# Performance work log

Measured on AMD Instinct MI355X. Metric: run time of the kernel, lower is better.

The kernel has to match this reference:

```python
import jax, jax.numpy as jnp
import numpy as np
import math

H = 1024  # hidden_dim
NH = 16   # num_heads
HD = H // NH  # head_dim = 64
B, S, C = 2, 2048, 256  # batch, seq_len, cond_len
EPS = 1e-5


def layernorm(x, g, b):
    m = jnp.mean(x, axis=-1, keepdims=True)
    v = jnp.var(x, axis=-1, keepdims=True)
    return (x - m) * jax.lax.rsqrt(v + EPS) * g + b


def apply_rope(x, freqs):
    # x: [b, s, h, d], freqs broadcastable to [b, s, h, d//2]
    cos, sin = jnp.cos(freqs), jnp.sin(freqs)
    x1, x2 = jnp.split(x, 2, axis=-1)
    return jnp.concatenate([x1 * cos - x2 * sin, x2 * cos + x1 * sin], axis=-1)


def setup_inputs() -> dict:
    key = jax.random.key(0)
    ks = jax.random.split(key, 16)
    sc = 0.02
    x = jax.random.normal(ks[0], (B, S, H), jnp.float32)
    # rope freqs: positions * inv_freq over half head dim
    inv_freq = 1.0 / (10000.0 ** (jnp.arange(HD // 2, dtype=jnp.float32) / (HD // 2)))
    rope_freqs = (jnp.arange(S, dtype=jnp.float32)[:, None] * inv_freq[None, :]).reshape(S, 1, HD // 2)
    # causal additive mask [1,1,S,S]
    causal = jnp.tril(jnp.ones((S, S), dtype=bool))
    attention_mask = jnp.where(causal, 0.0, -1e9).astype(jnp.float32)[None, None]
    conditioning = jax.random.normal(ks[1], (B, C, H), jnp.float32)
    conditioning_mask = jnp.zeros((B, 1, 1, C), jnp.float32)
    params = dict(
        ln1_g=jnp.ones((H,)), ln1_b=jnp.zeros((H,)),
        ln2_g=jnp.ones((H,)), ln2_b=jnp.zeros((H,)),
        lnc_g=jnp.ones((H,)), lnc_b=jnp.zeros((H,)),
        w_qkv=jax.random.normal(ks[2], (H, 3 * H)) * sc,
        w_out=jax.random.normal(ks[3], (H, H)) * sc, b_out=jnp.zeros((H,)),
        w_cq=jax.random.normal(ks[4], (H, H)) * sc,
        w_ckv=jax.random.normal(ks[5], (H, 2 * H)) * sc,
        w_cout=jax.random.normal(ks[6], (H, H)) * sc, b_cout=jnp.zeros((H,)),
        w_ff1=jax.random.normal(ks[7], (H, 4 * H)) * sc, b_ff1=jnp.zeros((4 * H,)),
        w_ff2=jax.random.normal(ks[8], (4 * H, H)) * sc, b_ff2=jnp.zeros((H,)),
    )
    return dict(x=x, rope_freqs=rope_freqs, attention_mask=attention_mask,
                conditioning=conditioning, conditioning_mask=conditioning_mask, **params)


def reference(x, rope_freqs, attention_mask, conditioning, conditioning_mask,
              ln1_g, ln1_b, ln2_g, ln2_b, lnc_g, lnc_b,
              w_qkv, w_out, b_out, w_cq, w_ckv, w_cout, b_cout,
              w_ff1, b_ff1, w_ff2, b_ff2):
    scale = 1.0 / math.sqrt(HD)
    # --- causal self-attention ---
    residual = x
    h = layernorm(x, ln1_g, ln1_b)
    qkv = h @ w_qkv  # [b,s,3H]
    q, k, v = jnp.split(qkv, 3, axis=-1)
    q = q.reshape(B, S, NH, HD)
    k = k.reshape(B, S, NH, HD)
    v = v.reshape(B, S, NH, HD)
    q = apply_rope(q, rope_freqs)
    k = apply_rope(k, rope_freqs)
    scores = jnp.einsum('bqhd,bkhd->bhqk', q, k) * scale + attention_mask
    attn = jax.nn.softmax(scores, axis=-1)
    out = jnp.einsum('bhqk,bkhd->bqhd', attn, v).reshape(B, S, H)
    x = residual + out @ w_out + b_out
    # --- cross-attention ---
    residual = x
    h = layernorm(x, lnc_g, lnc_b)
    q = (h @ w_cq).reshape(B, S, NH, HD)
    kv = conditioning @ w_ckv
    k, v = jnp.split(kv, 2, axis=-1)
    k = k.reshape(B, C, NH, HD)
    v = v.reshape(B, C, NH, HD)
    scores = jnp.einsum('bqhd,bkhd->bhqk', q, k) * scale + conditioning_mask
    attn = jax.nn.softmax(scores, axis=-1)
    out = jnp.einsum('bhqk,bkhd->bqhd', attn, v).reshape(B, S, H)
    x = residual + out @ w_cout + b_cout
    # --- FFN ---
    residual = x
    h = layernorm(x, ln2_g, ln2_b)
    h = jax.nn.gelu(h @ w_ff1 + b_ff1, approximate=False)
    x = residual + h @ w_ff2 + b_ff2
    return x
```

## Files before the change

kernel.cpp:

```cpp
#include <hip/hip_runtime.h>

#define HDIM   1024
#define NHEADS 16
#define HEADD  64
#define BATCH  2
#define SEQ    2048
#define CLEN   256
#define NROWS  (BATCH*SEQ)
#define SCALE  0.125f
#define LOG2E  1.44269504088896f

typedef __bf16 bf16x8 __attribute__((ext_vector_type(8)));
typedef float  f32x4  __attribute__((ext_vector_type(4)));

__device__ __forceinline__ unsigned short f2bf(float f) {
  union { __bf16 b; unsigned short u; } x;
  x.b = (__bf16)f;
  return x.u;
}
__device__ __forceinline__ float bf2f(unsigned short u) {
  union { unsigned int u; float f; } x; x.u = ((unsigned int)u) << 16;
  return x.f;
}

__device__ __forceinline__ void gl2lds16(const unsigned short* g, unsigned short* l) {
  __builtin_amdgcn_global_load_lds(
      (const __attribute__((address_space(1))) unsigned int*)g,
      (__attribute__((address_space(3))) unsigned int*)l, 16, 0, 0);
}

template<int VM> __device__ __forceinline__ void wait_vm_barrier() {
  if constexpr (VM == 0)      asm volatile("s_waitcnt vmcnt(0)\n\ts_barrier" ::: "memory");
  else if constexpr (VM == 2) asm volatile("s_waitcnt vmcnt(2)\n\ts_barrier" ::: "memory");
  else if constexpr (VM == 3) asm volatile("s_waitcnt vmcnt(3)\n\ts_barrier" ::: "memory");
  else if constexpr (VM == 4) asm volatile("s_waitcnt vmcnt(4)\n\ts_barrier" ::: "memory");
  else                        asm volatile("s_waitcnt vmcnt(6)\n\ts_barrier" ::: "memory");
}
__device__ __forceinline__ void bar_only() { asm volatile("s_barrier" ::: "memory"); }

struct CastTab { const float* s[8]; unsigned short* d[8]; };

__global__ __launch_bounds__(256)
void cast_fused(CastTab tab) {
  __shared__ float t[64][68];
  const int bid = blockIdx.x;
  const int tid = threadIdx.x;
  int w, base, K, N;
  if      (bid < 768)  { w = 0; base = 0;    K = 1024; N = 3072; }
  else if (bid < 1024) { w = 1; base = 768;  K = 1024; N = 1024; }
  else if (bid < 1280) { w = 2; base = 1024; K = 1024; N = 1024; }
  else if (bid < 1792) { w = 3; base = 1280; K = 1024; N = 2048; }
  else if (bid < 2048) { w = 4; base = 1792; K = 1024; N = 1024; }
  else if (bid < 3072) { w = 5; base = 2048; K = 1024; N = 4096; }
  else if (bid < 4096) { w = 6; base = 3072; K = 4096; N = 1024; }
  else                 { w = 7; base = 4096; K = 0;    N = 0;    }
  if (w == 7) {
    const float* in = tab.s[7];
    unsigned short* out = tab.d[7];
    int i = (bid - base) * 256 + tid;
    float4 a = ((const float4*)in)[2 * i], bq = ((const float4*)in)[2 * i + 1];
    unsigned short us[8] = { f2bf(a.x),  f2bf(a.y),  f2bf(a.z),  f2bf(a.w),
                             f2bf(bq.x), f2bf(bq.y), f2bf(bq.z), f2bf(bq.w) };
    ((uint4*)out)[i] = *(uint4*)us;
    return;
  }
  const float* in = tab.s[w];
  unsigned short* out = tab.d[w];
  const int lb = bid - base;
  const int tilesX = N >> 6;
  const int bx = lb % tilesX, by = lb / tilesX;
  const int kb = by * 64, nb = bx * 64;
  const int r = tid >> 4, c = (tid & 15) * 4;
#pragma unroll
  for (int i = 0; i < 4; ++i) {
    float4 v = *(const float4*)(in + (size_t)(kb + r + i * 16) * N + nb + c);
    t[r + i * 16][c]     = v.x;
    t[r + i * 16][c + 1] = v.y;
    t[r + i * 16][c + 2] = v.z;
    t[r + i * 16][c + 3] = v.w;
  }
  __syncthreads();
  const int nr = tid >> 3, kc = (tid & 7) * 8;
#pragma unroll
  for (int i = 0; i < 2; ++i) {
    unsigned short us[8];
#pragma unroll
    for (int j = 0; j < 8; ++j) us[j] = f2bf(t[kc + j][nr + i * 32]);
    *(uint4*)(out + (size_t)(nb + nr + i * 32) * K + kb + kc) = *(uint4*)us;
  }
}

__global__ __launch_bounds__(256)
void vtrans_kernel(const unsigned short* __restrict__ in, int str, int voff, int rows,
                   unsigned short* __restrict__ out) {
  __shared__ unsigned short t[64][72];
  const int h = blockIdx.y & (NHEADS - 1), b = blockIdx.y >> 4;
  const int s0 = blockIdx.x * 64;
  const int tid = threadIdx.x;
  const int r = tid >> 2, c = (tid & 3) * 16;
  const unsigned short* src = in + (size_t)(b * rows + s0 + r) * str + voff + h * 64 + c;
  *(uint4*)(&t[r][c])     = *(const uint4*)(src);
  *(uint4*)(&t[r][c + 8]) = *(const uint4*)(src + 8);
  __syncthreads();
  const int d = tid >> 2, sc = (tid & 3) * 16;
  unsigned short tmp[16];
#pragma unroll
  for (int i = 0; i < 16; ++i) tmp[i] = t[sc + i][d];
  unsigned short* dst = out + ((size_t)(b * NHEADS + h) * 64 + d) * rows + s0 + sc;
  *(uint4*)(dst)     = *(uint4*)(tmp);
  *(uint4*)(dst + 8) = *(uint4*)(tmp + 8);
}

__global__ __launch_bounds__(256)
void layernorm_kernel(const float* __restrict__ x, const float* __restrict__ g,
                      const float* __restrict__ b, unsigned short* __restrict__ out) {
  int row = blockIdx.x;
  const float4 v = ((const float4*)(x + (size_t)row * HDIM))[threadIdx.x];
  float s  = v.x + v.y + v.z + v.w;
  float sq = v.x*v.x + v.y*v.y + v.z*v.z + v.w*v.w;
  for (int o = 32; o; o >>= 1) { s += __shfl_xor(s, o); sq += __shfl_xor(sq, o); }
  __shared__ float rs[4], rq[4];
  int wave = threadIdx.x >> 6;
  if ((threadIdx.x & 63) == 0) { rs[wave] = s; rq[wave] = sq; }
  __syncthreads();
  s  = rs[0] + rs[1] + rs[2] + rs[3];
  sq = rq[0] + rq[1] + rq[2] + rq[3];
  float mean = s * (1.f/HDIM);
  float var  = sq * (1.f/HDIM) - mean*mean;
  float rstd = rsqrtf(var + 1e-5f);
  float4 gg = ((const float4*)g)[threadIdx.x];
  float4 bb = ((const float4*)b)[threadIdx.x];
  ushort4 o;
  o.x = f2bf((v.x - mean) * rstd * gg.x + bb.x);
  o.y = f2bf((v.y - mean) * rstd * gg.y + bb.y);
  o.z = f2bf((v.z - mean) * rstd * gg.z + bb.z);
  o.w = f2bf((v.w - mean) * rstd * gg.w + bb.w);
  ((ushort4*)(out + (size_t)row * HDIM))[threadIdx.x] = o;
}

template<int TBM, int TBN, int DEPTH, bool BIAS, bool RES, bool GELU_, bool OUTBF>
__global__ __launch_bounds__(512)
void gemm_bt(const unsigned short* __restrict__ A, const unsigned short* __restrict__ Bt,
             const float* __restrict__ bias, const float* __restrict__ res,
             void* __restrict__ out, int M, int N, int K) {
  constexpr int MR = TBM / 32;
  constexpr int NR = TBN / 64;
  constexpr int AIS = TBM / 64;
  constexpr int BIS = TBN / 64;
  constexpr int LOADS = AIS + BIS;
  constexpr int NBUF = DEPTH + 1;
  __shared__ unsigned short Al[NBUF][TBM * 64];
  __shared__ unsigned short Bl[NBUF][TBN * 64];
  const int tid  = threadIdx.x;
  const int wave = tid >> 6, lane = tid & 63;
  const int wr = wave >> 2, wc = wave & 3;
  const int nwg = gridDim.x * gridDim.y;
  int lin = blockIdx.y * gridDim.x + blockIdx.x;
  lin = (lin & 7) * (nwg >> 3) + (lin >> 3);
  const int m0 = (lin / gridDim.x) * TBM, n0 = (lin % gridDim.x) * TBN;
  const int lrow = lane & 15, hi = lane >> 4;
  const int rx = lrow & 7;

  f32x4 acc[MR][NR] = {};

  const int trow = tid >> 3, pslot = tid & 7;
  const int lcol = (pslot ^ (trow & 7)) * 8;
  const unsigned short* ga = A  + (size_t)(m0 + trow) * K + lcol;
  const unsigned short* gb = Bt + (size_t)(n0 + trow) * K + lcol;
  const int ldst = trow * 64 + pslot * 8;
  const int nt = K >> 6;

  auto stage = [&](int buf, int t) {
    const int k = t << 6;
#pragma unroll
    for (int i = 0; i < AIS; ++i)
      gl2lds16(ga + (size_t)i * 64 * K + k, Al[buf] + ldst + i * 64 * 64);
#pragma unroll
    for (int i = 0; i < BIS; ++i)
      gl2lds16(gb + (size_t)i * 64 * K + k, Bl[buf] + ldst + i * 64 * 64);
  };
  auto compute = [&](int c) {
#pragma unroll
    for (int kk = 0; kk < 2; ++kk) {
      const int cslot = ((kk << 2) | hi);
      const int coff  = (cslot ^ rx) * 8;
      bf16x8 af[MR], bfr[NR];
#pragma unroll
      for (int m = 0; m < MR; ++m)
        af[m] = *(const bf16x8*)(Al[c] + (wr*(TBM/2) + m*16 + lrow) * 64 + coff);
#pragma unroll
      for (int n = 0; n < NR; ++n)
        bfr[n] = *(const bf16x8*)(Bl[c] + (wc*(TBN/4) + n*16 + lrow) * 64 + coff);
#pragma unroll
      for (int m = 0; m < MR; ++m)
#pragma unroll
        for (int n = 0; n < NR; ++n)
          acc[m][n] = __builtin_amdgcn_mfma_f32_16x16x32_bf16(af[m], bfr[n], acc[m][n], 0, 0, 0);
    }
  };

  stage(0, 0);
  if constexpr (DEPTH == 2) stage(1, 1);
  int cur = 0;
  for (int t = 0; t < nt - DEPTH; ++t) {
    int nb = cur + DEPTH; if (nb >= NBUF) nb -= NBUF;
    stage(nb, t + DEPTH);
    wait_vm_barrier<DEPTH * LOADS>();
    compute(cur);
    bar_only();
    cur = (cur + 1 == NBUF) ? 0 : cur + 1;
  }
  if constexpr (DEPTH == 2) {
    wait_vm_barrier<LOADS>();
    compute(cur);
    bar_only();
    cur = (cur + 1 == NBUF) ? 0 : cur + 1;
  }
  wait_vm_barrier<0>();
  compute(cur);

#pragma unroll
  for (int m = 0; m < MR; ++m)
#pragma unroll
    for (int n = 0; n < NR; ++n)
#pragma unroll
      for (int r = 0; r < 4; ++r) {
        int row = m0 + wr*(TBM/2) + m*16 + hi * 4 + r;
        int col = n0 + wc*(TBN/4) + n*16 + lrow;
        float v = acc[m][n][r];
        if (BIAS)  v += bias[col];
        if (GELU_) v = 0.5f * v * (1.0f + erff(v * 0.70710678118654752f));
        if (RES)   v += res[(size_t)row * N + col];
        if (OUTBF) ((unsigned short*)out)[(size_t)row * N + col] = f2bf(v);
        else       ((float*)out)[(size_t)row * N + col] = v;
      }
}

__global__ void rope_kernel(unsigned short* __restrict__ qkv, const float* __restrict__ freqs) {
  int idx = blockIdx.x * 256 + threadIdx.x;
  int d = idx & 31;
  int h = (idx >> 5) & 15;
  int row = idx >> 9;
  int s = row & (SEQ - 1);
  float f = freqs[s * 32 + d];
  float sn, cs;
  sincosf(f, &sn, &cs);
  size_t base = (size_t)row * 3072 + h * 64 + d;
  float x1 = bf2f(qkv[base]), x2 = bf2f(qkv[base + 32]);
  qkv[base]      = f2bf(x1 * cs - x2 * sn);
  qkv[base + 32] = f2bf(x2 * cs + x1 * sn);
  float y1 = bf2f(qkv[base + 1024]), y2 = bf2f(qkv[base + 1024 + 32]);
  qkv[base + 1024]      = f2bf(y1 * cs - y2 * sn);
  qkv[base + 1024 + 32] = f2bf(y2 * cs + y1 * sn);
}

__global__ __launch_bounds__(512)
void flash_attn_causal8(const unsigned short* __restrict__ qp, int qstr,
                        const unsigned short* __restrict__ kp, int kstr,
                        const unsigned short* __restrict__ vt,
                        unsigned short* __restrict__ outp) {
  __shared__ unsigned short Kl[2][64 * 64];
  __shared__ unsigned short Vl[2][64 * 64];
  __shared__ unsigned short Pl[8][16][72];

  const int id = blockIdx.y * gridDim.x + blockIdx.x;
  const int bh = (id & 7) * 4 + ((id >> 3) & 3);
  const int qpair = id >> 5;
  const int h = bh & (NHEADS - 1), b = bh >> 4;

  const int tid = threadIdx.x;
  const int wave = tid >> 6, lane = tid & 63;
  const int grp = wave >> 2, w4 = wave & 3;
  const int lo = lane & 15, hi = lane >> 4;
  const int NQB = SEQ / 64;
  const float SC2 = SCALE * LOG2E;
  float* mb = (float*)&Pl[0][0][0];

  bf16x8 onesf;
#pragma unroll
  for (int j = 0; j < 8; ++j) onesf[j] = (__bf16)1.0f;

  const unsigned short* vbase = vt + (size_t)(b * NHEADS + h) * 64 * SEQ;
  const int g256 = tid & 255;
  const int trow = g256 >> 3, pslot = g256 & 7;
  const int lcol = (pslot ^ (trow & 7)) * 8;
  const int ldst = g256 * 8;
  const int x7 = lo & 7;
  const int c0 = (hi ^ x7) * 8, c1 = ((hi + 4) ^ x7) * 8;

  for (int pass = 0; pass < 2; ++pass) {
    const int qblk = pass == 0 ? qpair : NQB - 1 - qpair;
    const int q0 = qblk * 64;
    const int qw = q0 + w4 * 16;

    bf16x8 qf[2];
    {
      const unsigned short* qb = qp + (size_t)(b * SEQ + qw + lo) * qstr + h * 64 + hi * 8;
      qf[0] = *(const bf16x8*)(qb);
      qf[1] = *(const bf16x8*)(qb + 32);
#pragma unroll
      for (int j = 0; j < 8; ++j) {
        qf[0][j] = (__bf16)((float)qf[0][j] * SC2);
        qf[1][j] = (__bf16)((float)qf[1][j] * SC2);
      }
    }

    f32x4 o_acc[4] = {};
    f32x4 l_acc = {};
    float mrow[4];
#pragma unroll
    for (int r = 0; r < 4; ++r) mrow[r] = -1e30f;

    const int T = qblk + 1;
    const int iters = (T + 1) >> 1;
    for (int it = 0; it < iters; ++it) {
      const int t = 2 * it + grp;
      const bool act = t < T;
      const int j0 = t * 64;
      if (act) {
        const unsigned short* ks = kp + (size_t)(b * SEQ + j0 + trow) * kstr + h * 64 + lcol;
        const unsigned short* vs = vbase + (size_t)trow * SEQ + j0 + lcol;
        gl2lds16(ks, Kl[grp] + ldst);
        gl2lds16(ks + (size_t)32 * kstr, Kl[grp] + ldst + 32 * 64);
        gl2lds16(vs, Vl[grp] + ldst);
        gl2lds16(vs + (size_t)32 * SEQ, Vl[grp] + ldst + 32 * 64);
      }
      __syncthreads();
      if (act) {
        const unsigned short* Kc = Kl[grp];
        const unsigned short* Vc = Vl[grp];
        f32x4 s[4] = {};
#pragma unroll
        for (int n = 0; n < 4; ++n) {
          bf16x8 b0 = *(const bf16x8*)(Kc + (n * 16 + lo) * 64 + c0);
          bf16x8 b1 = *(const bf16x8*)(Kc + (n * 16 + lo) * 64 + c1);
          s[n] = __builtin_amdgcn_mfma_f32_16x16x32_bf16(qf[0], b0, s[n], 0, 0, 0);
          s[n] = __builtin_amdgcn_mfma_f32_16x16x32_bf16(qf[1], b1, s[n], 0, 0, 0);
        }
        if (t == T - 1) {
#pragma unroll
          for (int n = 0; n < 4; ++n)
#pragma unroll
            for (int r = 0; r < 4; ++r)
              if (j0 + n * 16 + lo > qw + hi * 4 + r) s[n][r] = -1e30f;
        }
        float pr[4][4];
#pragma unroll
        for (int r = 0; r < 4; ++r) {
          float mx = fmaxf(fmaxf(s[0][r], s[1][r]), fmaxf(s[2][r], s[3][r]));
          mx = fmaxf(mx, __shfl_xor(mx, 1));
          mx = fmaxf(mx, __shfl_xor(mx, 2));
          mx = fmaxf(mx, __shfl_xor(mx, 4));
          mx = fmaxf(mx, __shfl_xor(mx, 8));
          const float mnew = fmaxf(mrow[r], mx);
          const float corr = exp2f(mrow[r] - mnew);
          mrow[r] = mnew;
          l_acc[r] *= corr;
#pragma unroll
          for (int n = 0; n < 4; ++n)
            pr[n][r] = exp2f(s[n][r] - mnew);
#pragma unroll
          for (int n2 = 0; n2 < 4; ++n2) o_acc[n2][r] *= corr;
        }
#pragma unroll
        for (int n = 0; n < 4; ++n)
#pragma unroll
          for (int r = 0; r < 4; ++r)
            Pl[wave][hi * 4 + r][n * 16 + lo] = f2bf(pr[n][r]);

        bf16x8 pa0 = *(const bf16x8*)(&Pl[wave][lo][hi * 8]);
        bf16x8 pa1 = *(const bf16x8*)(&Pl[wave][lo][32 + hi * 8]);
        l_acc = __builtin_amdgcn_mfma_f32_16x16x32_bf16(pa0, onesf, l_acc, 0, 0, 0);
        l_acc = __builtin_amdgcn_mfma_f32_16x16x32_bf16(pa1, onesf, l_acc, 0, 0, 0);
#pragma unroll
        for (int n = 0; n < 4; ++n) {
          bf16x8 vb0 = *(const bf16x8*)(Vc + (n * 16 + lo) * 64 + c0);
          bf16x8 vb1 = *(const bf16x8*)(Vc + (n * 16 + lo) * 64 + c1);
          o_acc[n] = __builtin_amdgcn_mfma_f32_16x16x32_bf16(pa0, vb0, o_acc[n], 0, 0, 0);
          o_acc[n] = __builtin_amdgcn_mfma_f32_16x16x32_bf16(pa1, vb1, o_acc[n], 0, 0, 0);
        }
      }
      __syncthreads();
    }

    unsigned short* ob = outp + (size_t)(b * SEQ + qw) * HDIM + h * 64;
#pragma unroll
    for (int half = 0; half < 2; ++half) {
      __syncthreads();
      if (grp == 1) {
        float* dst = mb + (w4 * 64 + lane) * 13;
#pragma unroll
        for (int rr = 0; rr < 2; ++rr) {
          int r = half * 2 + rr;
          dst[rr * 6]     = mrow[r];
          dst[rr * 6 + 1] = l_acc[r];
#pragma unroll
          for (int n = 0; n < 4; ++n) dst[rr * 6 + 2 + n] = o_acc[n][r];
        }
      }
      __syncthreads();
      if (grp == 0) {
        const float* s1 = mb + (w4 * 64 + lane) * 13;
#pragma unroll
        for (int rr = 0; rr < 2; ++rr) {
          int r = half * 2 + rr;
          float m1 = s1[rr * 6], l1 = s1[rr * 6 + 1];
          float M  = fmaxf(mrow[r], m1);
          float c0f = exp2f(mrow[r] - M), c1f = exp2f(m1 - M);
          float inv = 1.f / (l_acc[r] * c0f + l1 * c1f);
#pragma unroll
          for (int n = 0; n < 4; ++n) {
            float o = o_acc[n][r] * c0f + s1[rr * 6 + 2 + n] * c1f;
            ob[(size_t)(hi * 4 + r) * HDIM + n * 16 + lo] = f2bf(o * inv);
          }
        }
      }
    }
    __syncthreads();
  }
}

__global__ __launch_bounds__(256)
void flash_attn_cross(const unsigned short* __restrict__ qp, int qstr,
                      const unsigned short* __restrict__ kp, int kstr,
                      const unsigned short* __restrict__ vt,
                      int kvrows,
                      unsigned short* __restrict__ outp) {
  __shared__ unsigned short Kl[2][64 * 64];
  __shared__ unsigned short Vl[2][64 * 64];
  __shared__ unsigned short Pl[4][16][72];

  const int id = blockIdx.y * gridDim.x + blockIdx.x;
  const int bh = (id & 7) * 4 + ((id >> 3) & 3);
  const int qblk = id >> 5;
  const int h = bh & (NHEADS - 1), b = bh >> 4;

  const int tid = threadIdx.x;
  const int wave = tid >> 6, lane = tid & 63;
  const int lo = lane & 15, hi = lane >> 4;
  const float SC2 = SCALE * LOG2E;

  bf16x8 onesf;
#pragma unroll
  for (int j = 0; j < 8; ++j) onesf[j] = (__bf16)1.0f;

  const unsigned short* vbase = vt + (size_t)(b * NHEADS + h) * 64 * kvrows;
  const int trow = tid >> 3, pslot = tid & 7;
  const int lcol = (pslot ^ (trow & 7)) * 8;
  const int ldst = tid * 8;
  const int x7 = lo & 7;
  const int c0 = (hi ^ x7) * 8, c1 = ((hi + 4) ^ x7) * 8;

  const int qw = qblk * 64 + wave * 16;

  bf16x8 qf[2];
  {
    const unsigned short* qb = qp + (size_t)(b * SEQ + qw + lo) * qstr + h * 64 + hi * 8;
    qf[0] = *(const bf16x8*)(qb);
    qf[1] = *(const bf16x8*)(qb + 32);
#pragma unroll
    for (int j = 0; j < 8; ++j) {
      qf[0][j] = (__bf16)((float)qf[0][j] * SC2);
      qf[1][j] = (__bf16)((float)qf[1][j] * SC2);
    }
  }

  f32x4 o_acc[4] = {};
  f32x4 l_acc = {};
  float mrow[4];
#pragma unroll
  for (int r = 0; r < 4; ++r) mrow[r] = -1e30f;

  auto stageKV = [&](int buf, int t) {
    const int j = t * 64;
    const unsigned short* ks = kp + (size_t)(b * kvrows + j + trow) * kstr + h * 64 + lcol;
    const unsigned short* vs = vbase + (size_t)trow * kvrows + j + lcol;
    gl2lds16(ks, Kl[buf] + ldst);
    gl2lds16(ks + (size_t)32 * kstr, Kl[buf] + ldst + 32 * 64);
    gl2lds16(vs, Vl[buf] + ldst);
    gl2lds16(vs + (size_t)32 * kvrows, Vl[buf] + ldst + 32 * 64);
  };
  auto computeTile = [&](int c) {
    const unsigned short* Kc = Kl[c];
    const unsigned short* Vc = Vl[c];
    f32x4 s[4] = {};
#pragma unroll
    for (int n = 0; n < 4; ++n) {
      bf16x8 b0 = *(const bf16x8*)(Kc + (n * 16 + lo) * 64 + c0);
      bf16x8 b1 = *(const bf16x8*)(Kc + (n * 16 + lo) * 64 + c1);
      s[n] = __builtin_amdgcn_mfma_f32_16x16x32_bf16(qf[0], b0, s[n], 0, 0, 0);
      s[n] = __builtin_amdgcn_mfma_f32_16x16x32_bf16(qf[1], b1, s[n], 0, 0, 0);
    }
    float pr[4][4];
#pragma unroll
    for (int r = 0; r < 4; ++r) {
      float mx = fmaxf(fmaxf(s[0][r], s[1][r]), fmaxf(s[2][r], s[3][r]));
      mx = fmaxf(mx, __shfl_xor(mx, 1));
      mx = fmaxf(mx, __shfl_xor(mx, 2));
      mx = fmaxf(mx, __shfl_xor(mx, 4));
      mx = fmaxf(mx, __shfl_xor(mx, 8));
      const float mnew = fmaxf(mrow[r], mx);
      const float corr = exp2f(mrow[r] - mnew);
      mrow[r] = mnew;
      l_acc[r] *= corr;
#pragma unroll
      for (int n = 0; n < 4; ++n)
        pr[n][r] = exp2f(s[n][r] - mnew);
#pragma unroll
      for (int n2 = 0; n2 < 4; ++n2) o_acc[n2][r] *= corr;
    }
#pragma unroll
    for (int n = 0; n < 4; ++n)
#pragma unroll
      for (int r = 0; r < 4; ++r)
        Pl[wave][hi * 4 + r][n * 16 + lo] = f2bf(pr[n][r]);
    bf16x8 pa0 = *(const bf16x8*)(&Pl[wave][lo][hi * 8]);
    bf16x8 pa1 = *(const bf16x8*)(&Pl[wave][lo][32 + hi * 8]);
    l_acc = __builtin_amdgcn_mfma_f32_16x16x32_bf16(pa0, onesf, l_acc, 0, 0, 0);
    l_acc = __builtin_amdgcn_mfma_f32_16x16x32_bf16(pa1, onesf, l_acc, 0, 0, 0);
#pragma unroll
    for (int n = 0; n < 4; ++n) {
      bf16x8 vb0 = *(const bf16x8*)(Vc + (n * 16 + lo) * 64 + c0);
      bf16x8 vb1 = *(const bf16x8*)(Vc + (n * 16 + lo) * 64 + c1);
      o_acc[n] = __builtin_amdgcn_mfma_f32_16x16x32_bf16(pa0, vb0, o_acc[n], 0, 0, 0);
      o_acc[n] = __builtin_amdgcn_mfma_f32_16x16x32_bf16(pa1, vb1, o_acc[n], 0, 0, 0);
    }
  };

  const int T = kvrows / 64;
  stageKV(0, 0);
  int cur = 0;
  for (int t = 0; t < T - 1; ++t) {
    stageKV(cur ^ 1, t + 1);
    wait_vm_barrier<4>();
    computeTile(cur);
    bar_only();
    cur ^= 1;
  }
  wait_vm_barrier<0>();
  computeTile(cur);

  unsigned short* ob = outp + (size_t)(b * SEQ + qw) * HDIM + h * 64;
#pragma unroll
  for (int r = 0; r < 4; ++r) {
    const float inv = 1.f / l_acc[r];
#pragma unroll
    for (int n = 0; n < 4; ++n)
      ob[(size_t)(hi * 4 + r) * HDIM + n * 16 + lo] = f2bf(o_acc[n][r] * inv);
  }
}

extern "C" void kernel_launch(void* const* d_in, const int* in_sizes, int n_in,
                              void* d_out, int out_size, void* d_ws, size_t ws_size,
                              hipStream_t stream) {
  const float* x      = (const float*)d_in[0];
  const float* rfreq  = (const float*)d_in[1];
  const float* cond   = (const float*)d_in[3];
  const float* ln1_g  = (const float*)d_in[5];
  const float* ln1_b  = (const float*)d_in[6];
  const float* ln2_g  = (const float*)d_in[7];
  const float* ln2_b  = (const float*)d_in[8];
  const float* lnc_g  = (const float*)d_in[9];
  const float* lnc_b  = (const float*)d_in[10];
  const float* w_qkv  = (const float*)d_in[11];
  const float* w_out  = (const float*)d_in[12];
  const float* b_out  = (const float*)d_in[13];
  const float* w_cq   = (const float*)d_in[14];
  const float* w_ckv  = (const float*)d_in[15];
  const float* w_cout = (const float*)d_in[16];
  const float* b_cout = (const float*)d_in[17];
  const float* w_ff1  = (const float*)d_in[18];
  const float* b_ff1  = (const float*)d_in[19];
  const float* w_ff2  = (const float*)d_in[20];
  const float* b_ff2  = (const float*)d_in[21];

  char* ws = (char*)d_ws;
  size_t off = 0;
  auto alloc = [&](size_t bytes) { size_t r = off; off += (bytes + 255) & ~(size_t)255; return r; };
  unsigned short* wt_qkv  = (unsigned short*)(ws + alloc((size_t)3072*1024*2));
  unsigned short* wt_out  = (unsigned short*)(ws + alloc((size_t)1024*1024*2));
  unsigned short* wt_cq   = (unsigned short*)(ws + alloc((size_t)1024*1024*2));
  unsigned short* wt_ckv  = (unsigned short*)(ws + alloc((size_t)2048*1024*2));
  unsigned short* wt_cout = (unsigned short*)(ws + alloc((size_t)1024*1024*2));
  unsigned short* wt_ff1  = (unsigned short*)(ws + alloc((size_t)4096*1024*2));
  unsigned short* wt_ff2  = (unsigned short*)(ws + alloc((size_t)1024*4096*2));
  unsigned short* condb   = (unsigned short*)(ws + alloc((size_t)512*1024*2));
  unsigned short* hbuf    = (unsigned short*)(ws + alloc((size_t)NROWS*1024*2));
  unsigned short* big     = (unsigned short*)(ws + alloc((size_t)NROWS*4096*2));
  unsigned short* attnb   = (unsigned short*)(ws + alloc((size_t)NROWS*1024*2));
  float*          x1      = (float*)(ws + alloc((size_t)NROWS*1024*4));
  unsigned short* kvc     = (unsigned short*)(ws + alloc((size_t)512*2048*2));
  unsigned short* vts     = (unsigned short*)(ws + alloc((size_t)BATCH*NHEADS*64*SEQ*2));
  unsigned short* vtc     = (unsigned short*)(ws + alloc((size_t)BATCH*NHEADS*64*CLEN*2));
  float*          outf    = (float*)d_out;

  CastTab tab;
  tab.s[0] = w_qkv;  tab.d[0] = wt_qkv;
  tab.s[1] = w_out;  tab.d[1] = wt_out;
  tab.s[2] = w_cq;   tab.d[2] = wt_cq;
  tab.s[3] = w_ckv;  tab.d[3] = wt_ckv;
  tab.s[4] = w_cout; tab.d[4] = wt_cout;
  tab.s[5] = w_ff1;  tab.d[5] = wt_ff1;
  tab.s[6] = w_ff2;  tab.d[6] = wt_ff2;
  tab.s[7] = cond;   tab.d[7] = condb;
  cast_fused<<<4352, 256, 0, stream>>>(tab);

  layernorm_kernel<<<NROWS, 256, 0, stream>>>(x, ln1_g, ln1_b, hbuf);
  gemm_bt<128,128,1,false,false,false,true><<<dim3(3072/128, NROWS/128), 512, 0, stream>>>(
      hbuf, wt_qkv, nullptr, nullptr, big, NROWS, 3072, 1024);
  rope_kernel<<<(NROWS*NHEADS*32)/256, 256, 0, stream>>>(big, rfreq);
  vtrans_kernel<<<dim3(SEQ/64, BATCH*NHEADS), 256, 0, stream>>>(big, 3072, 2048, SEQ, vts);
  flash_attn_causal8<<<dim3(SEQ/64/2, BATCH*NHEADS), 512, 0, stream>>>(
      big, 3072, big + 1024, 3072, vts, attnb);
  gemm_bt<128,64,2,true,true,false,false><<<dim3(1024/64, NROWS/128), 512, 0, stream>>>(
      attnb, wt_out, b_out, x, x1, NROWS, 1024, 1024);

  layernorm_kernel<<<NROWS, 256, 0, stream>>>(x1, lnc_g, lnc_b, hbuf);
  gemm_bt<128,64,2,false,false,false,true><<<dim3(1024/64, NROWS/128), 512, 0, stream>>>(
      hbuf, wt_cq, nullptr, nullptr, big, NROWS, 1024, 1024);
  gemm_bt<64,64,2,false,false,false,true><<<dim3(2048/64, 512/64), 512, 0, stream>>>(
      condb, wt_ckv, nullptr, nullptr, kvc, 512, 2048, 1024);
  vtrans_kernel<<<dim3(CLEN/64, BATCH*NHEADS), 256, 0, stream>>>(kvc, 2048, 1024, CLEN, vtc);
  flash_attn_cross<<<dim3(SEQ/64, BATCH*NHEADS), 256, 0, stream>>>(
      big, 1024, kvc, 2048, vtc, CLEN, attnb);
  gemm_bt<128,64,2,true,true,false,false><<<dim3(1024/64, NROWS/128), 512, 0, stream>>>(
      attnb, wt_cout, b_cout, x1, outf, NROWS, 1024, 1024);

  layernorm_kernel<<<NROWS, 256, 0, stream>>>(outf, ln2_g, ln2_b, hbuf);
  gemm_bt<128,128,1,true,false,true,true><<<dim3(4096/128, NROWS/128), 512, 0, stream>>>(
      hbuf, wt_ff1, b_ff1, nullptr, big, NROWS, 4096, 1024);
  gemm_bt<128,64,2,true,true,false,false><<<dim3(1024/64, NROWS/128), 512, 0, stream>>>(
      big, wt_ff2, b_ff2, outf, outf, NROWS, 1024, 4096);
}
```

Before: 316.3 us.

## Fuse Q RoPE into causal attention and store mid residual in bf16

The separate RoPE pass now rotates only K. The rotation of Q moves into the causal flash-attention kernel's Q load, using sincos on the frequency table. The intermediate residual after self-attention is stored as bf16 instead of fp32, with a new bf16 layernorm and a bf16-residual path in the GEMM epilogue. This is meant to cut global memory traffic in the rope, out-projection, layernorm and cout kernels. The cost is extra sincos work per attention block (done twice per block because of the two passes) and lower precision in the residual stream.

```diff
diff --git a/kernel.cpp b/kernel.cpp
--- a/kernel.cpp
+++ b/kernel.cpp
@@ -138,10 +138,38 @@
   ((ushort4*)(out + (size_t)row * HDIM))[threadIdx.x] = o;
 }
 
-template<int TBM, int TBN, int DEPTH, bool BIAS, bool RES, bool GELU_, bool OUTBF>
+__global__ __launch_bounds__(256)
+void layernorm_bf16_kernel(const unsigned short* __restrict__ x, const float* __restrict__ g,
+                           const float* __restrict__ b, unsigned short* __restrict__ out) {
+  int row = blockIdx.x;
+  ushort4 uv = ((const ushort4*)(x + (size_t)row * HDIM))[threadIdx.x];
+  float v0 = bf2f(uv.x), v1 = bf2f(uv.y), v2 = bf2f(uv.z), v3 = bf2f(uv.w);
+  float s  = v0 + v1 + v2 + v3;
+  float sq = v0*v0 + v1*v1 + v2*v2 + v3*v3;
+  for (int o = 32; o; o >>= 1) { s += __shfl_xor(s, o); sq += __shfl_xor(sq, o); }
+  __shared__ float rs[4], rq[4];
+  int wave = threadIdx.x >> 6;
+  if ((threadIdx.x & 63) == 0) { rs[wave] = s; rq[wave] = sq; }
+  __syncthreads();
+  s  = rs[0] + rs[1] + rs[2] + rs[3];
+  sq = rq[0] + rq[1] + rq[2] + rq[3];
+  float mean = s * (1.f/HDIM);
+  float var  = sq * (1.f/HDIM) - mean*mean;
+  float rstd = rsqrtf(var + 1e-5f);
+  float4 gg = ((const float4*)g)[threadIdx.x];
+  float4 bb = ((const float4*)b)[threadIdx.x];
+  ushort4 o;
+  o.x = f2bf((v0 - mean) * rstd * gg.x + bb.x);
+  o.y = f2bf((v1 - mean) * rstd * gg.y + bb.y);
+  o.z = f2bf((v2 - mean) * rstd * gg.z + bb.z);
+  o.w = f2bf((v3 - mean) * rstd * gg.w + bb.w);
+  ((ushort4*)(out + (size_t)row * HDIM))[threadIdx.x] = o;
+}
+
+template<int TBM, int TBN, int DEPTH, bool BIAS, bool RES, bool RESBF, bool GELU_, bool OUTBF>
 __global__ __launch_bounds__(512)
 void gemm_bt(const unsigned short* __restrict__ A, const unsigned short* __restrict__ Bt,
-             const float* __restrict__ bias, const float* __restrict__ res,
+             const float* __restrict__ bias, const void* __restrict__ res,
              void* __restrict__ out, int M, int N, int K) {
   constexpr int MR = TBM / 32;
   constexpr int NR = TBN / 64;
@@ -230,13 +258,16 @@
         float v = acc[m][n][r];
         if (BIAS)  v += bias[col];
         if (GELU_) v = 0.5f * v * (1.0f + erff(v * 0.70710678118654752f));
-        if (RES)   v += res[(size_t)row * N + col];
+        if (RES) {
+          if constexpr (RESBF) v += bf2f(((const unsigned short*)res)[(size_t)row * N + col]);
+          else                 v += ((const float*)res)[(size_t)row * N + col];
+        }
         if (OUTBF) ((unsigned short*)out)[(size_t)row * N + col] = f2bf(v);
         else       ((float*)out)[(size_t)row * N + col] = v;
       }
 }
 
-__global__ void rope_kernel(unsigned short* __restrict__ qkv, const float* __restrict__ freqs) {
+__global__ void rope_k_kernel(unsigned short* __restrict__ qkv, const float* __restrict__ freqs) {
   int idx = blockIdx.x * 256 + threadIdx.x;
   int d = idx & 31;
   int h = (idx >> 5) & 15;
@@ -245,19 +276,17 @@
   float f = freqs[s * 32 + d];
   float sn, cs;
   sincosf(f, &sn, &cs);
-  size_t base = (size_t)row * 3072 + h * 64 + d;
-  float x1 = bf2f(qkv[base]), x2 = bf2f(qkv[base + 32]);
-  qkv[base]      = f2bf(x1 * cs - x2 * sn);
-  qkv[base + 32] = f2bf(x2 * cs + x1 * sn);
-  float y1 = bf2f(qkv[base + 1024]), y2 = bf2f(qkv[base + 1024 + 32]);
-  qkv[base + 1024]      = f2bf(y1 * cs - y2 * sn);
-  qkv[base + 1024 + 32] = f2bf(y2 * cs + y1 * sn);
+  size_t base = (size_t)row * 3072 + h * 64 + d + 1024;
+  float y1 = bf2f(qkv[base]), y2 = bf2f(qkv[base + 32]);
+  qkv[base]      = f2bf(y1 * cs - y2 * sn);
+  qkv[base + 32] = f2bf(y2 * cs + y1 * sn);
 }
 
 __global__ __launch_bounds__(512)
 void flash_attn_causal8(const unsigned short* __restrict__ qp, int qstr,
                         const unsigned short* __restrict__ kp, int kstr,
                         const unsigned short* __restrict__ vt,
+                        const float* __restrict__ rfreq,
                         unsigned short* __restrict__ outp) {
   __shared__ unsigned short Kl[2][64 * 64];
   __shared__ unsigned short Vl[2][64 * 64];
@@ -298,10 +327,14 @@
       const unsigned short* qb = qp + (size_t)(b * SEQ + qw + lo) * qstr + h * 64 + hi * 8;
       qf[0] = *(const bf16x8*)(qb);
       qf[1] = *(const bf16x8*)(qb + 32);
+      const float* fr = rfreq + (size_t)(qw + lo) * 32 + hi * 8;
 #pragma unroll
       for (int j = 0; j < 8; ++j) {
-        qf[0][j] = (__bf16)((float)qf[0][j] * SC2);
-        qf[1][j] = (__bf16)((float)qf[1][j] * SC2);
+        float sn, cs;
+        sincosf(fr[j], &sn, &cs);
+        float x1 = (float)qf[0][j], x2 = (float)qf[1][j];
+        qf[0][j] = (__bf16)((x1 * cs - x2 * sn) * SC2);
+        qf[1][j] = (__bf16)((x2 * cs + x1 * sn) * SC2);
       }
     }
 
@@ -588,7 +621,7 @@
   unsigned short* hbuf    = (unsigned short*)(ws + alloc((size_t)NROWS*1024*2));
   unsigned short* big     = (unsigned short*)(ws + alloc((size_t)NROWS*4096*2));
   unsigned short* attnb   = (unsigned short*)(ws + alloc((size_t)NROWS*1024*2));
-  float*          x1      = (float*)(ws + alloc((size_t)NROWS*1024*4));
+  unsigned short* x1b     = (unsigned short*)(ws + alloc((size_t)NROWS*1024*2));
   unsigned short* kvc     = (unsigned short*)(ws + alloc((size_t)512*2048*2));
   unsigned short* vts     = (unsigned short*)(ws + alloc((size_t)BATCH*NHEADS*64*SEQ*2));
   unsigned short* vtc     = (unsigned short*)(ws + alloc((size_t)BATCH*NHEADS*64*CLEN*2));
@@ -606,29 +639,29 @@
   cast_fused<<<4352, 256, 0, stream>>>(tab);
 
   layernorm_kernel<<<NROWS, 256, 0, stream>>>(x, ln1_g, ln1_b, hbuf);
-  gemm_bt<128,128,1,false,false,false,true><<<dim3(3072/128, NROWS/128), 512, 0, stream>>>(
+  gemm_bt<128,128,1,false,false,false,false,true><<<dim3(3072/128, NROWS/128), 512, 0, stream>>>(
       hbuf, wt_qkv, nullptr, nullptr, big, NROWS, 3072, 1024);
-  rope_kernel<<<(NROWS*NHEADS*32)/256, 256, 0, stream>>>(big, rfreq);
+  rope_k_kernel<<<(NROWS*NHEADS*32)/256, 256, 0, stream>>>(big, rfreq);
   vtrans_kernel<<<dim3(SEQ/64, BATCH*NHEADS), 256, 0, stream>>>(big, 3072, 2048, SEQ, vts);
   flash_attn_causal8<<<dim3(SEQ/64/2, BATCH*NHEADS), 512, 0, stream>>>(
-      big, 3072, big + 1024, 3072, vts, attnb);
-  gemm_bt<128,64,2,true,true,false,false><<<dim3(1024/64, NROWS/128), 512, 0, stream>>>(
-      attnb, wt_out, b_out, x, x1, NROWS, 1024, 1024);
-
-  layernorm_kernel<<<NROWS, 256, 0, stream>>>(x1, lnc_g, lnc_b, hbuf);
-  gemm_bt<128,64,2,false,false,false,true><<<dim3(1024/64, NROWS/128), 512, 0, stream>>>(
+      big, 3072, big + 1024, 3072, vts, rfreq, attnb);
+  gemm_bt<128,64,2,true,true,false,false,true><<<dim3(1024/64, NROWS/128), 512, 0, stream>>>(
+      attnb, wt_out, b_out, x, x1b, NROWS, 1024, 1024);
+
+  layernorm_bf16_kernel<<<NROWS, 256, 0, stream>>>(x1b, lnc_g, lnc_b, hbuf);
+  gemm_bt<128,64,2,false,false,false,false,true><<<dim3(1024/64, NROWS/128), 512, 0, stream>>>(
       hbuf, wt_cq, nullptr, nullptr, big, NROWS, 1024, 1024);
-  gemm_bt<64,64,2,false,false,false,true><<<dim3(2048/64, 512/64), 512, 0, stream>>>(
+  gemm_bt<64,64,2,false,false,false,false,true><<<dim3(2048/64, 512/64), 512, 0, stream>>>(
       condb, wt_ckv, nullptr, nullptr, kvc, 512, 2048, 1024);
   vtrans_kernel<<<dim3(CLEN/64, BATCH*NHEADS), 256, 0, stream>>>(kvc, 2048, 1024, CLEN, vtc);
   flash_attn_cross<<<dim3(SEQ/64, BATCH*NHEADS), 256, 0, stream>>>(
       big, 1024, kvc, 2048, vtc, CLEN, attnb);
-  gemm_bt<128,64,2,true,true,false,false><<<dim3(1024/64, NROWS/128), 512, 0, stream>>>(
-      attnb, wt_cout, b_cout, x1, outf, NROWS, 1024, 1024);
+  gemm_bt<128,64,2,true,true,true,false,false><<<dim3(1024/64, NROWS/128), 512, 0, stream>>>(
+      attnb, wt_cout, b_cout, x1b, outf, NROWS, 1024, 1024);
 
   layernorm_kernel<<<NROWS, 256, 0, stream>>>(outf, ln2_g, ln2_b, hbuf);
-  gemm_bt<128,128,1,true,false,true,true><<<dim3(4096/128, NROWS/128), 512, 0, stream>>>(
+  gemm_bt<128,128,1,true,false,false,true,true><<<dim3(4096/128, NROWS/128), 512, 0, stream>>>(
       hbuf, wt_ff1, b_ff1, nullptr, big, NROWS, 4096, 1024);
-  gemm_bt<128,64,2,true,true,false,false><<<dim3(1024/64, NROWS/128), 512, 0, stream>>>(
+  gemm_bt<128,64,2,true,true,false,false,false><<<dim3(1024/64, NROWS/128), 512, 0, stream>>>(
       big, wt_ff2, b_ff2, outf, outf, NROWS, 1024, 4096);
 }
```

New measurement: 317.6 us. No clear change (+0.4%).
